# Optimization experiments

Measured on AMD Instinct MI355X. Metric: run time of the kernel, lower is better.

The kernel has to match this reference:

```python
import jax, jax.numpy as jnp
import numpy as np

NUM_HEADS = 8


def setup_inputs() -> dict:
    key = jax.random.key(0)
    k1, k2 = jax.random.split(key)
    C, B, N, D = 3, 2, 4096, 512
    x = jax.random.normal(k1, (C, B, N, D), dtype=jnp.float32)
    proj_w = jax.random.normal(k2, (D, D), dtype=jnp.float32) * (D ** -0.5)
    proj_b = jnp.zeros((D,), dtype=jnp.float32)
    return {"x": x, "proj_w": proj_w, "proj_b": proj_b}


def reference(x, proj_w, proj_b):
    C, B, N, D = x.shape
    H = NUM_HEADS
    hd = D // H
    scale = hd ** -0.5
    # [3, B, N, H, hd] -> [3, B, H, N, hd]
    xh = x.reshape(C, B, N, H, hd).transpose(0, 1, 3, 2, 4)
    q, k, v = xh[0], xh[1], xh[2]
    # attention scores [B, H, N, N]
    attn = jnp.einsum('bhqd,bhkd->bhqk', q, k) * scale
    attn = jax.nn.softmax(attn, axis=-1)
    out = jnp.einsum('bhqk,bhkd->bhqd', attn, v)  # [B, H, N, hd]
    out = out.transpose(0, 2, 1, 3).reshape(B, N, D)
    # nn.Linear: y = x @ W^T + b
    return out @ proj_w.T + proj_b
```

## Files before the change

### kernel.cpp

```cpp
#include <hip/hip_runtime.h>
#include <hip/hip_bf16.h>

typedef __attribute__((ext_vector_type(8))) short short8;
typedef __attribute__((ext_vector_type(4))) float f32x4;
typedef __attribute__((ext_vector_type(16))) float f32x16;
typedef __attribute__((ext_vector_type(4))) unsigned uint4v;

#define MFMA16(a, b, c) __builtin_amdgcn_mfma_f32_16x16x32_bf16((a), (b), (c), 0, 0, 0)
#define MFMA32(a, b, c) __builtin_amdgcn_mfma_f32_32x32x16_bf16((a), (b), (c), 0, 0, 0)

#define NB 2
#define NSEQ 4096
#define DMODEL 512
#define NH 8
#define HD 64
#define CSTRIDE (NB * NSEQ * DMODEL)

#define QSCALE 0.18033688011112042f

static __device__ __forceinline__ unsigned short f2bf(float f) {
    unsigned u = __builtin_bit_cast(unsigned, f);
    u += 0x7fffu + ((u >> 16) & 1u);
    return (unsigned short)(u >> 16);
}

static __device__ __forceinline__ short8 cvt8(float4 a, float4 b) {
    short8 r;
    r[0] = (short)f2bf(a.x); r[1] = (short)f2bf(a.y);
    r[2] = (short)f2bf(a.z); r[3] = (short)f2bf(a.w);
    r[4] = (short)f2bf(b.x); r[5] = (short)f2bf(b.y);
    r[6] = (short)f2bf(b.z); r[7] = (short)f2bf(b.w);
    return r;
}

static __device__ __forceinline__ unsigned cvt_pk_bf16(float lo, float hi) {
    unsigned r;
    asm("v_cvt_pk_bf16_f32 %0, %1, %2" : "=v"(r) : "v"(lo), "v"(hi));
    return r;
}

static __device__ __forceinline__ void gload_lds16(const void* g, void* l) {
    __builtin_amdgcn_global_load_lds(
        (const __attribute__((address_space(1))) void*)g,
        (__attribute__((address_space(3))) void*)l, 16, 0, 0);
}

__global__ __launch_bounds__(256)
void qk_convert(const float* __restrict__ x, unsigned short* __restrict__ Qbf,
                unsigned short* __restrict__ Kbf) {
    int cid = blockIdx.x * 256 + threadIdx.x;
    int d8 = cid & 63;
    int n = (cid >> 6) & 4095;
    int b = (cid >> 18) & 1;
    int c = cid >> 19;
    const float* src = x + (size_t)c * CSTRIDE + ((size_t)(b * 4096 + n)) * 512 + d8 * 8;
    float4 a0 = *reinterpret_cast<const float4*>(src);
    float4 a1 = *reinterpret_cast<const float4*>(src + 4);
    float sc = c ? 1.0f : QSCALE;
    a0.x *= sc; a0.y *= sc; a0.z *= sc; a0.w *= sc;
    a1.x *= sc; a1.y *= sc; a1.z *= sc; a1.w *= sc;
    unsigned short* dst = (c ? Kbf : Qbf) +
        (((size_t)(b * 8 + (d8 >> 3)) * 4096 + n) * 64 + (d8 & 7) * 8);
    *reinterpret_cast<short8*>(dst) = cvt8(a0, a1);
}

__global__ __launch_bounds__(256)
void v_transpose(const float* __restrict__ x, unsigned short* __restrict__ Vt) {
    __shared__ __attribute__((aligned(16))) unsigned short T[64 * 66];
    unsigned* T32 = reinterpret_cast<unsigned*>(T);

    const int tid = threadIdx.x;
    const int bh = blockIdx.y;
    const int b = bh >> 3, h = bh & 7;
    const int n0 = blockIdx.x * 64;

#pragma unroll
    for (int j = 0; j < 2; ++j) {
        int cid = tid + 256 * j;
        int ni = cid >> 3;
        int d0 = (cid & 7) * 8;
        const float* src = x + (size_t)2 * CSTRIDE +
            ((size_t)(b * 4096 + n0 + ni)) * 512 + h * 64 + d0;
        float4 a0 = *reinterpret_cast<const float4*>(src);
        float4 a1 = *reinterpret_cast<const float4*>(src + 4);
        short8 v = cvt8(a0, a1);
#pragma unroll
        for (int k = 0; k < 4; ++k) {
            unsigned pk = (unsigned)(unsigned short)v[2 * k] |
                          ((unsigned)(unsigned short)v[2 * k + 1] << 16);
            T32[ni * 33 + (d0 >> 1) + k] = pk;
        }
    }
    __syncthreads();

#pragma unroll
    for (int j = 0; j < 2; ++j) {
        int cid = tid + 256 * j;
        int di = cid >> 3;
        int k0 = (cid & 7) * 8;
        short8 o;
#pragma unroll
        for (int k = 0; k < 8; ++k) o[k] = (short)T[(k0 + k) * 66 + di];
        unsigned short* dst = Vt + ((size_t)(bh * 64 + di)) * 4096 + n0 + k0;
        *reinterpret_cast<short8*>(dst) = o;
    }
}

__global__ __launch_bounds__(256)
void w_convert(const float* __restrict__ W, unsigned short* __restrict__ Wbf) {
    int cid = blockIdx.x * 256 + threadIdx.x;
    int d8 = cid & 63;
    int row = cid >> 6;
    const float* src = W + (size_t)row * 512 + d8 * 8;
    float4 a0 = *reinterpret_cast<const float4*>(src);
    float4 a1 = *reinterpret_cast<const float4*>(src + 4);
    *reinterpret_cast<short8*>(Wbf + (size_t)row * 512 + d8 * 8) = cvt8(a0, a1);
}

#define SMEM_BYTES 65536

__global__ __launch_bounds__(256, 2)
void attn_kernel(const unsigned short* __restrict__ Qbf,
                 const unsigned short* __restrict__ Kbf,
                 const unsigned short* __restrict__ Vt,
                 unsigned short* __restrict__ Obf) {
    __shared__ __attribute__((aligned(16))) unsigned char SMEM[SMEM_BYTES];

    const int tid = threadIdx.x;
    const int lane = tid & 63;
    const int wv = tid >> 6;
    const int hi = lane >> 5;
    const int l5 = lane & 31;
    const int half = wv >> 1;
    const int qs = wv & 1;
    const int w2 = wv & 1;

    const int bh = blockIdx.y;
    const int b = bh >> 3, h = bh & 7;
    const int qbase = blockIdx.x * 128 + qs * 64;

    const unsigned short* Qh = Qbf + (size_t)bh * NSEQ * HD;
    const unsigned short* Kh = Kbf + (size_t)bh * NSEQ * HD;
    const unsigned short* Vh = Vt + (size_t)bh * HD * NSEQ;

    char* K_base = (char*)SMEM + half * 32768;

    short8 qf[2][4];
#pragma unroll
    for (int u = 0; u < 2; ++u)
#pragma unroll
        for (int c = 0; c < 4; ++c)
            qf[u][c] = *reinterpret_cast<const short8*>(
                Qh + (size_t)(qbase + u * 32 + l5) * HD + c * 16 + hi * 8);

    f32x16 zero16;
#pragma unroll
    for (int r = 0; r < 16; ++r) zero16[r] = 0.f;

    f32x16 oacc[2][2];
#pragma unroll
    for (int u = 0; u < 2; ++u)
#pragma unroll
        for (int db = 0; db < 2; ++db) oacc[u][db] = zero16;
    float l_run[2] = {0.f, 0.f};

    const int kt0 = half * 32;
    const int swz = (l5 & 7) << 4;

    const int lrow = lane >> 3;
    const int lelem = ((lane & 7) * 8) ^ (lrow * 8);

    {
        char* Kb = K_base;
        char* Vb = K_base + 8192;
#pragma unroll
        for (int i = 0; i < 4; ++i) {
            int j = w2 * 4 + i;
            int row = j * 8 + lrow;
            gload_lds16(Kh + (size_t)(kt0 * 64 + row) * HD + lelem, Kb + j * 1024);
            gload_lds16(Vh + (size_t)row * NSEQ + kt0 * 64 + lelem, Vb + j * 1024);
        }
    }
    __syncthreads();

    int cur = 0;
    for (int step = 0; step < 32; ++step) {
        if (step < 31) {
            int nt = kt0 + step + 1;
            char* Kb = K_base + (cur ^ 1) * 16384;
            char* Vb = Kb + 8192;
#pragma unroll
            for (int i = 0; i < 4; ++i) {
                int j = w2 * 4 + i;
                int row = j * 8 + lrow;
                gload_lds16(Kh + (size_t)(nt * 64 + row) * HD + lelem, Kb + j * 1024);
                gload_lds16(Vh + (size_t)row * NSEQ + nt * 64 + lelem, Vb + j * 1024);
            }
        }

        const char* K_lds = K_base + cur * 16384;
        const char* V_lds = K_lds + 8192;

        f32x16 st[2][2];
        __builtin_amdgcn_s_setprio(1);
#pragma unroll
        for (int kb = 0; kb < 2; ++kb) {
            int key = kb * 32 + l5;
            short8 kf0 = *reinterpret_cast<const short8*>(
                K_lds + ((key * 128 + 0 * 32 + hi * 16) ^ swz));
            f32x16 aA = MFMA32(kf0, qf[0][0], zero16);
            f32x16 aB = MFMA32(kf0, qf[1][0], zero16);
#pragma unroll
            for (int c = 1; c < 4; ++c) {
                short8 kf = *reinterpret_cast<const short8*>(
                    K_lds + ((key * 128 + c * 32 + hi * 16) ^ swz));
                aA = MFMA32(kf, qf[0][c], aA);
                aB = MFMA32(kf, qf[1][c], aB);
            }
            st[0][kb] = aA;
            st[1][kb] = aB;
        }
        __builtin_amdgcn_s_setprio(0);

#pragma unroll
        for (int u = 0; u < 2; ++u) {
#pragma unroll
            for (int kb = 0; kb < 2; ++kb)
#pragma unroll
                for (int r = 0; r < 16; ++r)
                    st[u][kb][r] = __builtin_amdgcn_exp2f(st[u][kb][r]);
            float s = 0.f;
#pragma unroll
            for (int r = 0; r < 16; ++r) s += st[u][0][r] + st[u][1][r];
            s += __shfl_xor(s, 32);
            l_run[u] += s;
        }

        short8 PA[2][4];
#pragma unroll
        for (int u = 0; u < 2; ++u)
#pragma unroll
            for (int kb = 0; kb < 2; ++kb)
#pragma unroll
                for (int ks = 0; ks < 2; ++ks) {
                    unsigned c0 = cvt_pk_bf16(st[u][kb][8 * ks + 0], st[u][kb][8 * ks + 1]);
                    unsigned c1 = cvt_pk_bf16(st[u][kb][8 * ks + 2], st[u][kb][8 * ks + 3]);
                    unsigned c2 = cvt_pk_bf16(st[u][kb][8 * ks + 4], st[u][kb][8 * ks + 5]);
                    unsigned c3 = cvt_pk_bf16(st[u][kb][8 * ks + 6], st[u][kb][8 * ks + 7]);
                    unsigned d0 = (unsigned)__shfl_xor((int)c0, 32);
                    unsigned d1 = (unsigned)__shfl_xor((int)c1, 32);
                    unsigned d2 = (unsigned)__shfl_xor((int)c2, 32);
                    unsigned d3 = (unsigned)__shfl_xor((int)c3, 32);
                    uint4v w;
                    w[0] = hi ? d2 : c0;
                    w[1] = hi ? d3 : c1;
                    w[2] = hi ? c2 : d0;
                    w[3] = hi ? c3 : d1;
                    PA[u][kb * 2 + ks] = __builtin_bit_cast(short8, w);
                }

        __builtin_amdgcn_s_setprio(1);
#pragma unroll
        for (int ch = 0; ch < 4; ++ch) {
#pragma unroll
            for (int db = 0; db < 2; ++db) {
                int d = db * 32 + l5;
                short8 vf = *reinterpret_cast<const short8*>(
                    V_lds + ((d * 128 + ch * 32 + hi * 16) ^ swz));
                oacc[0][db] = MFMA32(PA[0][ch], vf, oacc[0][db]);
                oacc[1][db] = MFMA32(PA[1][ch], vf, oacc[1][db]);
            }
        }
        __builtin_amdgcn_s_setprio(0);

        __syncthreads();
        cur ^= 1;
    }

    float* Xo = (float*)SMEM;
    float* Xl = (float*)(SMEM + 32768);

    if (half == 1) {
#pragma unroll
        for (int u = 0; u < 2; ++u) {
#pragma unroll
            for (int r = 0; r < 16; ++r) {
                int crow = (r & 3) + 8 * (r >> 2) + 4 * hi;
                int qloc = qs * 64 + u * 32 + crow;
                Xo[qloc * 64 + l5] = oacc[u][0][r];
                Xo[qloc * 64 + 32 + l5] = oacc[u][1][r];
            }
            if (hi == 0) Xl[qs * 64 + u * 32 + l5] = l_run[u];
        }
    }
    __syncthreads();
    if (half == 0) {
#pragma unroll
        for (int u = 0; u < 2; ++u) {
#pragma unroll
            for (int r = 0; r < 16; ++r) {
                int crow = (r & 3) + 8 * (r >> 2) + 4 * hi;
                int qloc = qs * 64 + u * 32 + crow;
                float l1 = Xl[qloc];
                float inv = 1.0f / (__shfl(l_run[u], crow) + l1);
                float v0 = oacc[u][0][r] + Xo[qloc * 64 + l5];
                float v1 = oacc[u][1][r] + Xo[qloc * 64 + 32 + l5];
                int qrow = qbase + u * 32 + crow;
                size_t obase = (size_t)(b * NSEQ + qrow) * DMODEL + h * HD;
                Obf[obase + l5] = f2bf(v0 * inv);
                Obf[obase + 32 + l5] = f2bf(v1 * inv);
            }
        }
    }
}

__global__ __launch_bounds__(256, 4)
void proj_kernel(const unsigned short* __restrict__ Obf, const unsigned short* __restrict__ Wbf,
                 const float* __restrict__ bias, float* __restrict__ out) {
    __shared__ __attribute__((aligned(16))) unsigned short W_lds[64 * 64];

    const int tid = threadIdx.x;
    const int lane = tid & 63;
    const int wv = tid >> 6;
    const int g = lane >> 4;
    const int l4 = lane & 15;

    const int bm = blockIdx.x;
    const int bn = blockIdx.y;

    f32x4 acc[4];
#pragma unroll
    for (int jt = 0; jt < 4; ++jt) acc[jt] = (f32x4){0.f, 0.f, 0.f, 0.f};

    for (int kc = 0; kc < DMODEL / 64; ++kc) {
#pragma unroll
        for (int j = 0; j < 2; ++j) {
            int cid = tid + 256 * j;
            int row = cid >> 3;
            int ee = (cid & 7) * 8;
            short8 wv8 = *reinterpret_cast<const short8*>(
                Wbf + (size_t)(bn * 64 + row) * DMODEL + kc * 64 + ee);
            int off = (row * 128 + ee * 2) ^ ((row & 7) << 4);
            *reinterpret_cast<short8*>((char*)W_lds + off) = wv8;
        }
        __syncthreads();

#pragma unroll
        for (int sub = 0; sub < 2; ++sub) {
            const unsigned short* ap =
                Obf + (size_t)(bm * 64 + wv * 16 + l4) * DMODEL + kc * 64 + sub * 32 + g * 8;
            short8 a = *reinterpret_cast<const short8*>(ap);
#pragma unroll
            for (int jt = 0; jt < 4; ++jt) {
                int jj = jt * 16 + l4;
                int off = (jj * 128 + (sub * 32 + g * 8) * 2) ^ ((jj & 7) << 4);
                short8 wb = *reinterpret_cast<const short8*>((const char*)W_lds + off);
                acc[jt] = MFMA16(a, wb, acc[jt]);
            }
        }
        __syncthreads();
    }

#pragma unroll
    for (int jt = 0; jt < 4; ++jt) {
        int jg = bn * 64 + jt * 16 + l4;
        float bj = bias[jg];
#pragma unroll
        for (int r = 0; r < 4; ++r) {
            int ig = bm * 64 + wv * 16 + g * 4 + r;
            out[(size_t)ig * DMODEL + jg] = acc[jt][r] + bj;
        }
    }
}

extern "C" void kernel_launch(void* const* d_in, const int* in_sizes, int n_in,
                              void* d_out, int out_size, void* d_ws, size_t ws_size,
                              hipStream_t stream) {
    const float* x = (const float*)d_in[0];
    const float* W = (const float*)d_in[1];
    const float* bias = (const float*)d_in[2];
    float* out = (float*)d_out;

    char* ws = (char*)d_ws;
    unsigned short* Obf = (unsigned short*)(ws);
    unsigned short* Qbf = (unsigned short*)(ws + (8u << 20));
    unsigned short* Kbf = (unsigned short*)(ws + (16u << 20));
    unsigned short* Vt = (unsigned short*)(ws + (24u << 20));
    unsigned short* Wbf = (unsigned short*)(ws + (32u << 20));

    qk_convert<<<4096, 256, 0, stream>>>(x, Qbf, Kbf);
    v_transpose<<<dim3(NSEQ / 64, NB * NH), 256, 0, stream>>>(x, Vt);
    w_convert<<<128, 256, 0, stream>>>(W, Wbf);

    dim3 gA(NSEQ / 128, NB * NH);
    attn_kernel<<<gA, 256, 0, stream>>>(Qbf, Kbf, Vt, Obf);

    dim3 gP(NB * NSEQ / 64, DMODEL / 64);
    proj_kernel<<<gP, 256, 0, stream>>>(Obf, Wbf, bias, out);
}
```

Baseline: 129.4 us.

## Fuse Q bf16 conversion into attention and use 512-thread blocks

Removes the separate Q conversion pass: the attention kernel now reads fp32 Q straight from the input, applies the softmax scale and converts to bf16 in registers, and the prep kernel only converts K. The attention block grows to 8 waves, each handling 32 query rows instead of 64, with K/V tile loads split across four waves per key half. This raises waves per CU and cuts per-wave register state and the prep traffic. In exchange, LDS reads of K/V fragments double per MFMA, and each block does more uncoalesced fp32 Q reads.

```diff
diff --git a/kernel.cpp b/kernel.cpp
--- a/kernel.cpp
+++ b/kernel.cpp
@@ -46,20 +46,15 @@
 }
 
 __global__ __launch_bounds__(256)
-void qk_convert(const float* __restrict__ x, unsigned short* __restrict__ Qbf,
-                unsigned short* __restrict__ Kbf) {
+void k_convert(const float* __restrict__ x, unsigned short* __restrict__ Kbf) {
     int cid = blockIdx.x * 256 + threadIdx.x;
     int d8 = cid & 63;
     int n = (cid >> 6) & 4095;
-    int b = (cid >> 18) & 1;
-    int c = cid >> 19;
-    const float* src = x + (size_t)c * CSTRIDE + ((size_t)(b * 4096 + n)) * 512 + d8 * 8;
+    int b = cid >> 18;
+    const float* src = x + (size_t)CSTRIDE + ((size_t)(b * 4096 + n)) * 512 + d8 * 8;
     float4 a0 = *reinterpret_cast<const float4*>(src);
     float4 a1 = *reinterpret_cast<const float4*>(src + 4);
-    float sc = c ? 1.0f : QSCALE;
-    a0.x *= sc; a0.y *= sc; a0.z *= sc; a0.w *= sc;
-    a1.x *= sc; a1.y *= sc; a1.z *= sc; a1.w *= sc;
-    unsigned short* dst = (c ? Kbf : Qbf) +
+    unsigned short* dst = Kbf +
         (((size_t)(b * 8 + (d8 >> 3)) * 4096 + n) * 64 + (d8 & 7) * 8);
     *reinterpret_cast<short8*>(dst) = cvt8(a0, a1);
 }
@@ -119,8 +114,8 @@
 
 #define SMEM_BYTES 65536
 
-__global__ __launch_bounds__(256, 2)
-void attn_kernel(const unsigned short* __restrict__ Qbf,
+__global__ __launch_bounds__(512, 4)
+void attn_kernel(const float* __restrict__ x,
                  const unsigned short* __restrict__ Kbf,
                  const unsigned short* __restrict__ Vt,
                  unsigned short* __restrict__ Obf) {
@@ -131,51 +126,51 @@
     const int wv = tid >> 6;
     const int hi = lane >> 5;
     const int l5 = lane & 31;
-    const int half = wv >> 1;
-    const int qs = wv & 1;
-    const int w2 = wv & 1;
+    const int half = wv >> 2;
+    const int p = wv & 3;
 
     const int bh = blockIdx.y;
     const int b = bh >> 3, h = bh & 7;
-    const int qbase = blockIdx.x * 128 + qs * 64;
-
-    const unsigned short* Qh = Qbf + (size_t)bh * NSEQ * HD;
+    const int qbase = blockIdx.x * 128 + p * 32;
+
     const unsigned short* Kh = Kbf + (size_t)bh * NSEQ * HD;
     const unsigned short* Vh = Vt + (size_t)bh * HD * NSEQ;
 
     char* K_base = (char*)SMEM + half * 32768;
 
-    short8 qf[2][4];
-#pragma unroll
-    for (int u = 0; u < 2; ++u)
-#pragma unroll
-        for (int c = 0; c < 4; ++c)
-            qf[u][c] = *reinterpret_cast<const short8*>(
-                Qh + (size_t)(qbase + u * 32 + l5) * HD + c * 16 + hi * 8);
+    short8 qf[4];
+#pragma unroll
+    for (int c = 0; c < 4; ++c) {
+        const float* qp = x + ((size_t)(b * 4096 + qbase + l5)) * 512 + h * 64 + c * 16 + hi * 8;
+        float4 a0 = *reinterpret_cast<const float4*>(qp);
+        float4 a1 = *reinterpret_cast<const float4*>(qp + 4);
+        a0.x *= QSCALE; a0.y *= QSCALE; a0.z *= QSCALE; a0.w *= QSCALE;
+        a1.x *= QSCALE; a1.y *= QSCALE; a1.z *= QSCALE; a1.w *= QSCALE;
+        qf[c] = cvt8(a0, a1);
+    }
 
     f32x16 zero16;
 #pragma unroll
     for (int r = 0; r < 16; ++r) zero16[r] = 0.f;
 
-    f32x16 oacc[2][2];
-#pragma unroll
-    for (int u = 0; u < 2; ++u)
-#pragma unroll
-        for (int db = 0; db < 2; ++db) oacc[u][db] = zero16;
-    float l_run[2] = {0.f, 0.f};
+    f32x16 oacc[2];
+    oacc[0] = zero16;
+    oacc[1] = zero16;
+    float l_run = 0.f;
 
     const int kt0 = half * 32;
     const int swz = (l5 & 7) << 4;
 
     const int lrow = lane >> 3;
     const int lelem = ((lane & 7) * 8) ^ (lrow * 8);
+    const int j0 = p * 2;
 
     {
         char* Kb = K_base;
         char* Vb = K_base + 8192;
 #pragma unroll
-        for (int i = 0; i < 4; ++i) {
-            int j = w2 * 4 + i;
+        for (int i = 0; i < 2; ++i) {
+            int j = j0 + i;
             int row = j * 8 + lrow;
             gload_lds16(Kh + (size_t)(kt0 * 64 + row) * HD + lelem, Kb + j * 1024);
             gload_lds16(Vh + (size_t)row * NSEQ + kt0 * 64 + lelem, Vb + j * 1024);
@@ -190,8 +185,8 @@
             char* Kb = K_base + (cur ^ 1) * 16384;
             char* Vb = Kb + 8192;
 #pragma unroll
-            for (int i = 0; i < 4; ++i) {
-                int j = w2 * 4 + i;
+            for (int i = 0; i < 2; ++i) {
+                int j = j0 + i;
                 int row = j * 8 + lrow;
                 gload_lds16(Kh + (size_t)(nt * 64 + row) * HD + lelem, Kb + j * 1024);
                 gload_lds16(Vh + (size_t)row * NSEQ + nt * 64 + lelem, Vb + j * 1024);
@@ -201,63 +196,57 @@
         const char* K_lds = K_base + cur * 16384;
         const char* V_lds = K_lds + 8192;
 
-        f32x16 st[2][2];
+        f32x16 st[2];
         __builtin_amdgcn_s_setprio(1);
 #pragma unroll
         for (int kb = 0; kb < 2; ++kb) {
             int key = kb * 32 + l5;
             short8 kf0 = *reinterpret_cast<const short8*>(
                 K_lds + ((key * 128 + 0 * 32 + hi * 16) ^ swz));
-            f32x16 aA = MFMA32(kf0, qf[0][0], zero16);
-            f32x16 aB = MFMA32(kf0, qf[1][0], zero16);
+            f32x16 a = MFMA32(kf0, qf[0], zero16);
 #pragma unroll
             for (int c = 1; c < 4; ++c) {
                 short8 kf = *reinterpret_cast<const short8*>(
                     K_lds + ((key * 128 + c * 32 + hi * 16) ^ swz));
-                aA = MFMA32(kf, qf[0][c], aA);
-                aB = MFMA32(kf, qf[1][c], aB);
-            }
-            st[0][kb] = aA;
-            st[1][kb] = aB;
+                a = MFMA32(kf, qf[c], a);
+            }
+            st[kb] = a;
         }
         __builtin_amdgcn_s_setprio(0);
 
 #pragma unroll
-        for (int u = 0; u < 2; ++u) {
-#pragma unroll
-            for (int kb = 0; kb < 2; ++kb)
-#pragma unroll
-                for (int r = 0; r < 16; ++r)
-                    st[u][kb][r] = __builtin_amdgcn_exp2f(st[u][kb][r]);
+        for (int kb = 0; kb < 2; ++kb)
+#pragma unroll
+            for (int r = 0; r < 16; ++r)
+                st[kb][r] = __builtin_amdgcn_exp2f(st[kb][r]);
+        {
             float s = 0.f;
 #pragma unroll
-            for (int r = 0; r < 16; ++r) s += st[u][0][r] + st[u][1][r];
+            for (int r = 0; r < 16; ++r) s += st[0][r] + st[1][r];
             s += __shfl_xor(s, 32);
-            l_run[u] += s;
-        }
-
-        short8 PA[2][4];
-#pragma unroll
-        for (int u = 0; u < 2; ++u)
-#pragma unroll
-            for (int kb = 0; kb < 2; ++kb)
-#pragma unroll
-                for (int ks = 0; ks < 2; ++ks) {
-                    unsigned c0 = cvt_pk_bf16(st[u][kb][8 * ks + 0], st[u][kb][8 * ks + 1]);
-                    unsigned c1 = cvt_pk_bf16(st[u][kb][8 * ks + 2], st[u][kb][8 * ks + 3]);
-                    unsigned c2 = cvt_pk_bf16(st[u][kb][8 * ks + 4], st[u][kb][8 * ks + 5]);
-                    unsigned c3 = cvt_pk_bf16(st[u][kb][8 * ks + 6], st[u][kb][8 * ks + 7]);
-                    unsigned d0 = (unsigned)__shfl_xor((int)c0, 32);
-                    unsigned d1 = (unsigned)__shfl_xor((int)c1, 32);
-                    unsigned d2 = (unsigned)__shfl_xor((int)c2, 32);
-                    unsigned d3 = (unsigned)__shfl_xor((int)c3, 32);
-                    uint4v w;
-                    w[0] = hi ? d2 : c0;
-                    w[1] = hi ? d3 : c1;
-                    w[2] = hi ? c2 : d0;
-                    w[3] = hi ? c3 : d1;
-                    PA[u][kb * 2 + ks] = __builtin_bit_cast(short8, w);
-                }
+            l_run += s;
+        }
+
+        short8 PA[4];
+#pragma unroll
+        for (int kb = 0; kb < 2; ++kb)
+#pragma unroll
+            for (int ks = 0; ks < 2; ++ks) {
+                unsigned c0 = cvt_pk_bf16(st[kb][8 * ks + 0], st[kb][8 * ks + 1]);
+                unsigned c1 = cvt_pk_bf16(st[kb][8 * ks + 2], st[kb][8 * ks + 3]);
+                unsigned c2 = cvt_pk_bf16(st[kb][8 * ks + 4], st[kb][8 * ks + 5]);
+                unsigned c3 = cvt_pk_bf16(st[kb][8 * ks + 6], st[kb][8 * ks + 7]);
+                unsigned d0 = (unsigned)__shfl_xor((int)c0, 32);
+                unsigned d1 = (unsigned)__shfl_xor((int)c1, 32);
+                unsigned d2 = (unsigned)__shfl_xor((int)c2, 32);
+                unsigned d3 = (unsigned)__shfl_xor((int)c3, 32);
+                uint4v w;
+                w[0] = hi ? d2 : c0;
+                w[1] = hi ? d3 : c1;
+                w[2] = hi ? c2 : d0;
+                w[3] = hi ? c3 : d1;
+                PA[kb * 2 + ks] = __builtin_bit_cast(short8, w);
+            }
 
         __builtin_amdgcn_s_setprio(1);
 #pragma unroll
@@ -267,8 +256,7 @@
                 int d = db * 32 + l5;
                 short8 vf = *reinterpret_cast<const short8*>(
                     V_lds + ((d * 128 + ch * 32 + hi * 16) ^ swz));
-                oacc[0][db] = MFMA32(PA[0][ch], vf, oacc[0][db]);
-                oacc[1][db] = MFMA32(PA[1][ch], vf, oacc[1][db]);
+                oacc[db] = MFMA32(PA[ch], vf, oacc[db]);
             }
         }
         __builtin_amdgcn_s_setprio(0);
@@ -282,34 +270,28 @@
 
     if (half == 1) {
 #pragma unroll
-        for (int u = 0; u < 2; ++u) {
-#pragma unroll
-            for (int r = 0; r < 16; ++r) {
-                int crow = (r & 3) + 8 * (r >> 2) + 4 * hi;
-                int qloc = qs * 64 + u * 32 + crow;
-                Xo[qloc * 64 + l5] = oacc[u][0][r];
-                Xo[qloc * 64 + 32 + l5] = oacc[u][1][r];
-            }
-            if (hi == 0) Xl[qs * 64 + u * 32 + l5] = l_run[u];
-        }
+        for (int r = 0; r < 16; ++r) {
+            int crow = (r & 3) + 8 * (r >> 2) + 4 * hi;
+            int qloc = p * 32 + crow;
+            Xo[qloc * 64 + l5] = oacc[0][r];
+            Xo[qloc * 64 + 32 + l5] = oacc[1][r];
+        }
+        if (hi == 0) Xl[p * 32 + l5] = l_run;
     }
     __syncthreads();
     if (half == 0) {
 #pragma unroll
-        for (int u = 0; u < 2; ++u) {
-#pragma unroll
-            for (int r = 0; r < 16; ++r) {
-                int crow = (r & 3) + 8 * (r >> 2) + 4 * hi;
-                int qloc = qs * 64 + u * 32 + crow;
-                float l1 = Xl[qloc];
-                float inv = 1.0f / (__shfl(l_run[u], crow) + l1);
-                float v0 = oacc[u][0][r] + Xo[qloc * 64 + l5];
-                float v1 = oacc[u][1][r] + Xo[qloc * 64 + 32 + l5];
-                int qrow = qbase + u * 32 + crow;
-                size_t obase = (size_t)(b * NSEQ + qrow) * DMODEL + h * HD;
-                Obf[obase + l5] = f2bf(v0 * inv);
-                Obf[obase + 32 + l5] = f2bf(v1 * inv);
-            }
+        for (int r = 0; r < 16; ++r) {
+            int crow = (r & 3) + 8 * (r >> 2) + 4 * hi;
+            int qloc = p * 32 + crow;
+            float l1 = Xl[qloc];
+            float inv = 1.0f / (__shfl(l_run, crow) + l1);
+            float v0 = oacc[0][r] + Xo[qloc * 64 + l5];
+            float v1 = oacc[1][r] + Xo[qloc * 64 + 32 + l5];
+            int qrow = qbase + crow;
+            size_t obase = (size_t)(b * NSEQ + qrow) * DMODEL + h * HD;
+            Obf[obase + l5] = f2bf(v0 * inv);
+            Obf[obase + 32 + l5] = f2bf(v1 * inv);
         }
     }
 }
@@ -383,17 +365,16 @@
 
     char* ws = (char*)d_ws;
     unsigned short* Obf = (unsigned short*)(ws);
-    unsigned short* Qbf = (unsigned short*)(ws + (8u << 20));
-    unsigned short* Kbf = (unsigned short*)(ws + (16u << 20));
-    unsigned short* Vt = (unsigned short*)(ws + (24u << 20));
-    unsigned short* Wbf = (unsigned short*)(ws + (32u << 20));
-
-    qk_convert<<<4096, 256, 0, stream>>>(x, Qbf, Kbf);
+    unsigned short* Kbf = (unsigned short*)(ws + (8u << 20));
+    unsigned short* Vt = (unsigned short*)(ws + (16u << 20));
+    unsigned short* Wbf = (unsigned short*)(ws + (24u << 20));
+
+    k_convert<<<2048, 256, 0, stream>>>(x, Kbf);
     v_transpose<<<dim3(NSEQ / 64, NB * NH), 256, 0, stream>>>(x, Vt);
     w_convert<<<128, 256, 0, stream>>>(W, Wbf);
 
     dim3 gA(NSEQ / 128, NB * NH);
-    attn_kernel<<<gA, 256, 0, stream>>>(Qbf, Kbf, Vt, Obf);
+    attn_kernel<<<gA, 512, 0, stream>>>(x, Kbf, Vt, Obf);
 
     dim3 gP(NB * NSEQ / 64, DMODEL / 64);
     proj_kernel<<<gP, 256, 0, stream>>>(Obf, Wbf, bias, out);
```

After: 124.3 us. 1.04x faster.
